# Kernel optimization log

Hardware: AMD Instinct MI355X
Metric: run time of the kernel (lower is better)

## Reference

```python
import jax, jax.numpy as jnp
import numpy as np

B, T, C, H = 2, 2048, 1024, 16

def setup_inputs() -> dict:
    key = jax.random.key(0)
    ks = jax.random.split(key, 6)
    s = 1.0 / np.sqrt(C)
    return {
        "x": jax.random.normal(ks[0], (B, T, C), jnp.float32),
        "Wq": jax.random.normal(ks[1], (C, C), jnp.float32) * s,
        "Wk": jax.random.normal(ks[2], (C, C), jnp.float32) * s,
        "Wv": jax.random.normal(ks[3], (C, C), jnp.float32) * s,
        "Wp": jax.random.normal(ks[4], (C, C), jnp.float32) * s,
        "bp": jnp.zeros((C,), jnp.float32),
    }

def reference(x, Wq, Wk, Wv, Wp, bp):
    b, t, c = x.shape
    hd = c // H  # head dim
    # Linear layers: torch nn.Linear computes x @ W.T
    def split_heads(y):
        return y.reshape(b, t, H, hd).transpose(0, 2, 1, 3)  # [B,H,T,hd]
    q = split_heads(x @ Wq.T)
    k = split_heads(x @ Wk.T)
    v = split_heads(x @ Wv.T)
    scale = hd ** -0.5
    wei = jnp.einsum('bhqd,bhkd->bhqk', q, k) * scale  # [B,H,T,T]
    causal = jnp.tril(jnp.ones((t, t), bool))
    wei = jnp.where(causal, wei, -jnp.inf)
    wei = jax.nn.softmax(wei, axis=-1)
    out = jnp.einsum('bhqk,bhkd->bhqd', wei, v)  # [B,H,T,hd]
    out = out.transpose(0, 2, 1, 3).reshape(b, t, c)
    return out @ Wp.T + bp
```

## Files before the change

### kernel.cpp

```cpp
#include <hip/hip_runtime.h>
#include <hip/hip_bf16.h>
#include <stdint.h>

#define B_ 2
#define T_ 2048
#define C_ 1024
#define H_ 16
#define HD_ 64
#define NTOK (B_*T_)

typedef __bf16 bf16;
typedef bf16 bf16x4 __attribute__((ext_vector_type(4)));
typedef bf16 bf16x8 __attribute__((ext_vector_type(8)));
typedef float f32x4 __attribute__((ext_vector_type(4)));

static __device__ __forceinline__ f32x4 mfma16(bf16x8 a, bf16x8 b, f32x4 c) {
  return __builtin_amdgcn_mfma_f32_16x16x32_bf16(a, b, c, 0, 0, 0);
}

static __device__ __forceinline__ void gload_lds16(const void* g, void* l) {
  __builtin_amdgcn_global_load_lds(
      (__attribute__((address_space(1))) void*)g,
      (__attribute__((address_space(3))) void*)l, 16, 0, 0);
}

static __device__ __forceinline__ uint32_t cvt_pk_bf16(float lo, float hi) {
  uint32_t r;
  asm("v_cvt_pk_bf16_f32 %0, %1, %2" : "=v"(r) : "v"(lo), "v"(hi));
  return r;
}

__global__ void cvt_all(const float* __restrict__ x,
                        const float* __restrict__ w0, const float* __restrict__ w1,
                        const float* __restrict__ w2, const float* __restrict__ w3,
                        bf16* __restrict__ xb,
                        bf16* __restrict__ d0, bf16* __restrict__ d1,
                        bf16* __restrict__ d2, bf16* __restrict__ d3) {
  const int i = blockIdx.x * 256 + threadIdx.x;
  const int y = blockIdx.y;
  const float* src;
  bf16* dst;
  size_t off4 = 0;
  if (y < 4) {
    src = x; dst = xb; off4 = (size_t)y << 18;
  } else if (y == 4) { src = w0; dst = d0; }
  else if (y == 5)   { src = w1; dst = d1; }
  else if (y == 6)   { src = w2; dst = d2; }
  else               { src = w3; dst = d3; }
  float4 v = reinterpret_cast<const float4*>(src)[off4 + i];
  bf16x4 o;
  o.x = (bf16)v.x; o.y = (bf16)v.y; o.z = (bf16)v.z; o.w = (bf16)v.w;
  reinterpret_cast<bf16x4*>(dst)[off4 + i] = o;
}

__global__ __launch_bounds__(256) void qkv_gemm(
    const bf16* __restrict__ X,
    const bf16* __restrict__ Wq, const bf16* __restrict__ Wk, const bf16* __restrict__ Wv,
    bf16* __restrict__ Q, bf16* __restrict__ K, bf16* __restrict__ VT) {
  __shared__ bf16 As[128 * 32];
  __shared__ bf16 Bs[128 * 32];
  const int z = blockIdx.z;
  const bf16* W = (z == 0) ? Wq : (z == 1) ? Wk : Wv;
  const int n0 = blockIdx.x * 128;
  const int o0 = blockIdx.y * 128;
  const int tid = threadIdx.x;
  const int lane = tid & 63;
  const int w = tid >> 6;
  const int wr = w >> 1, wc = w & 1;
  const int l15 = lane & 15, lhi = lane >> 4;

  f32x4 acc[4][4] = {};

  const int ca = tid;
  const int cb = tid + 256;
  const int rowa = ca >> 2, cola = (ca & 3) * 8;
  const int rowb = cb >> 2, colb = (cb & 3) * 8;

  for (int k0 = 0; k0 < C_; k0 += 32) {
    __syncthreads();
    gload_lds16(X + (size_t)(n0 + rowa) * C_ + k0 + cola, (char*)As + ca * 16);
    gload_lds16(X + (size_t)(n0 + rowb) * C_ + k0 + colb, (char*)As + cb * 16);
    gload_lds16(W + (size_t)(o0 + rowa) * C_ + k0 + cola, (char*)Bs + ca * 16);
    gload_lds16(W + (size_t)(o0 + rowb) * C_ + k0 + colb, (char*)Bs + cb * 16);
    __syncthreads();
    bf16x8 a[4], b[4];
#pragma unroll
    for (int m = 0; m < 4; m++)
      a[m] = *reinterpret_cast<const bf16x8*>(&As[(wr * 64 + m * 16 + l15) * 32 + lhi * 8]);
#pragma unroll
    for (int n = 0; n < 4; n++)
      b[n] = *reinterpret_cast<const bf16x8*>(&Bs[(wc * 64 + n * 16 + l15) * 32 + lhi * 8]);
#pragma unroll
    for (int m = 0; m < 4; m++)
#pragma unroll
      for (int n = 0; n < 4; n++)
        acc[m][n] = mfma16(a[m], b[n], acc[m][n]);
  }

  const float QSCALE = 0.125f * 1.44269504f;
#pragma unroll
  for (int m = 0; m < 4; m++) {
#pragma unroll
    for (int n = 0; n < 4; n++) {
#pragma unroll
      for (int r = 0; r < 4; r++) {
        int tok = n0 + wr * 64 + m * 16 + lhi * 4 + r;
        int o = o0 + wc * 64 + n * 16 + l15;
        int bb = tok >> 11, t = tok & (T_ - 1);
        int h = o >> 6, d = o & 63;
        float v = acc[m][n][r];
        if (z == 0) {
          Q[((size_t)(bb * H_ + h) * T_ + t) * HD_ + d] = (bf16)(v * QSCALE);
        } else if (z == 1) {
          K[((size_t)(bb * H_ + h) * T_ + t) * HD_ + d] = (bf16)v;
        } else {
          VT[((size_t)(bb * H_ + h) * HD_ + d) * T_ + t] = (bf16)v;
        }
      }
    }
  }
}

__global__ __launch_bounds__(256, 3) void attn_kernel(
    const bf16* __restrict__ Q, const bf16* __restrict__ K,
    const bf16* __restrict__ VT, bf16* __restrict__ att) {
  __shared__ bf16 Kt[2][64 * 64];
  __shared__ bf16 Vt[2][64 * 64];
  __shared__ bf16 P[4][32][72];
  const int tid = threadIdx.x;
  const int lane = tid & 63;
  const int w = tid >> 6;
  const int l15 = lane & 15, lhi = lane >> 4;
  const int bh = blockIdx.x;
  const int b = bh >> 4, h = bh & 15;
  const int by = (int)blockIdx.y;
  const int qt = (by < 8) ? (15 - by) : (by - 8);
  const int qw0 = qt * 128 + w * 32;
  const bf16* Qb = Q + (size_t)bh * T_ * HD_;
  const bf16* Kb = K + (size_t)bh * T_ * HD_;
  const bf16* Vb = VT + (size_t)bh * HD_ * T_;

  bf16x8 q[2][2];
#pragma unroll
  for (int m = 0; m < 2; m++)
#pragma unroll
    for (int kk = 0; kk < 2; kk++)
      q[m][kk] = *reinterpret_cast<const bf16x8*>(
          &Qb[(size_t)(qw0 + m * 16 + l15) * HD_ + kk * 32 + lhi * 8]);

  f32x4 o_acc[2][4] = {};
  float lsum[2] = {0.f, 0.f};

  const int nt = 2 * qt + 2;

  const int c0 = tid, c1 = tid + 256;
  const int r0 = c0 >> 3, x0 = (c0 & 7) ^ (r0 & 7);
  const int r1 = c1 >> 3, x1 = (c1 & 7) ^ (r1 & 7);

#define STAGE(tt, bb)                                                                \
  do {                                                                               \
    int kv = (tt) * 64;                                                              \
    gload_lds16(Kb + (size_t)(kv + r0) * HD_ + x0 * 8, (char*)&Kt[bb][0] + c0 * 16); \
    gload_lds16(Kb + (size_t)(kv + r1) * HD_ + x1 * 8, (char*)&Kt[bb][0] + c1 * 16); \
    gload_lds16(Vb + (size_t)r0 * T_ + kv + x0 * 8, (char*)&Vt[bb][0] + c0 * 16);    \
    gload_lds16(Vb + (size_t)r1 * T_ + kv + x1 * 8, (char*)&Vt[bb][0] + c1 * 16);    \
  } while (0)

  STAGE(0, 0);
  __syncthreads();
  int cur = 0;

  for (int it = 0; it < nt; ++it) {
    const int kv0 = it * 64;
    if (it + 1 < nt) STAGE(it + 1, cur ^ 1);

    if (kv0 <= qw0 + 31) {
      f32x4 s[2][4] = {};
#pragma unroll
      for (int n = 0; n < 4; n++) {
        const int krow = n * 16 + l15;
#pragma unroll
        for (int kk = 0; kk < 2; kk++) {
          const int kx = (kk * 4 + lhi) ^ (l15 & 7);
          bf16x8 kf = *reinterpret_cast<const bf16x8*>(
              (const char*)&Kt[cur][0] + krow * 128 + kx * 16);
          s[0][n] = mfma16(kf, q[0][kk], s[0][n]);
          s[1][n] = mfma16(kf, q[1][kk], s[1][n]);
        }
      }

      if (kv0 + 63 > qw0) {
#pragma unroll
        for (int m = 0; m < 2; m++) {
          const int qrow = qw0 + m * 16 + l15;
#pragma unroll
          for (int n = 0; n < 4; n++) {
            const int key = kv0 + n * 16 + lhi * 4;
#pragma unroll
            for (int r = 0; r < 4; r++) {
              if (key + r > qrow) s[m][n][r] = -1e30f;
            }
          }
        }
      }
#pragma unroll
      for (int m = 0; m < 2; m++) {
        char* pw = (char*)&P[w][m * 16 + l15][0];
#pragma unroll
        for (int n = 0; n < 4; n++) {
          float p0 = __builtin_amdgcn_exp2f(s[m][n][0]);
          float p1 = __builtin_amdgcn_exp2f(s[m][n][1]);
          float p2 = __builtin_amdgcn_exp2f(s[m][n][2]);
          float p3 = __builtin_amdgcn_exp2f(s[m][n][3]);
          lsum[m] += (p0 + p1) + (p2 + p3);
          uint32_t lo = cvt_pk_bf16(p0, p1);
          uint32_t hi = cvt_pk_bf16(p2, p3);
          *reinterpret_cast<uint2*>(pw + (4 * n + lhi) * 8) = make_uint2(lo, hi);
        }
      }
      bf16x8 pa[2][2];
#pragma unroll
      for (int m = 0; m < 2; m++)
#pragma unroll
        for (int kk = 0; kk < 2; kk++)
          pa[m][kk] = *reinterpret_cast<const bf16x8*>(
              (const char*)&P[w][m * 16 + l15][0] + kk * 64 + lhi * 16);
#pragma unroll
      for (int n = 0; n < 4; n++) {
        const int vrow = n * 16 + l15;
#pragma unroll
        for (int kk = 0; kk < 2; kk++) {
          const int vx = (kk * 4 + lhi) ^ (l15 & 7);
          bf16x8 vf = *reinterpret_cast<const bf16x8*>(
              (const char*)&Vt[cur][0] + vrow * 128 + vx * 16);
          o_acc[0][n] = mfma16(pa[0][kk], vf, o_acc[0][n]);
          o_acc[1][n] = mfma16(pa[1][kk], vf, o_acc[1][n]);
        }
      }
    }
    __syncthreads();
    cur ^= 1;
  }
#undef STAGE

  float lred[2];
#pragma unroll
  for (int m = 0; m < 2; m++) {
    float v = lsum[m];
    v += __shfl_xor(v, 16);
    v += __shfl_xor(v, 32);
    lred[m] = v;
  }
#pragma unroll
  for (int m = 0; m < 2; m++) {
#pragma unroll
    for (int r = 0; r < 4; r++) {
      float rs = __shfl(lred[m], (lane & 48) + lhi * 4 + r);
      float li = 1.f / rs;
      int t = qw0 + m * 16 + lhi * 4 + r;
#pragma unroll
      for (int n = 0; n < 4; n++) {
        int d = n * 16 + l15;
        att[((size_t)(b * T_ + t) * H_ + h) * HD_ + d] = (bf16)(o_acc[m][n][r] * li);
      }
    }
  }
}

__global__ __launch_bounds__(256) void proj_gemm(
    const bf16* __restrict__ A, const bf16* __restrict__ Wp,
    const float* __restrict__ bp, float* __restrict__ out) {
  __shared__ bf16 As[128 * 32];
  __shared__ bf16 Bs[128 * 32];
  const int n0 = blockIdx.x * 128;
  const int o0 = blockIdx.y * 128;
  const int tid = threadIdx.x;
  const int lane = tid & 63;
  const int w = tid >> 6;
  const int wr = w >> 1, wc = w & 1;
  const int l15 = lane & 15, lhi = lane >> 4;

  f32x4 acc[4][4] = {};

  const int ca = tid;
  const int cb = tid + 256;
  const int rowa = ca >> 2, cola = (ca & 3) * 8;
  const int rowb = cb >> 2, colb = (cb & 3) * 8;

  for (int k0 = 0; k0 < C_; k0 += 32) {
    __syncthreads();
    gload_lds16(A + (size_t)(n0 + rowa) * C_ + k0 + cola, (char*)As + ca * 16);
    gload_lds16(A + (size_t)(n0 + rowb) * C_ + k0 + colb, (char*)As + cb * 16);
    gload_lds16(Wp + (size_t)(o0 + rowa) * C_ + k0 + cola, (char*)Bs + ca * 16);
    gload_lds16(Wp + (size_t)(o0 + rowb) * C_ + k0 + colb, (char*)Bs + cb * 16);
    __syncthreads();
    bf16x8 a[4], b[4];
#pragma unroll
    for (int m = 0; m < 4; m++)
      a[m] = *reinterpret_cast<const bf16x8*>(&As[(wr * 64 + m * 16 + l15) * 32 + lhi * 8]);
#pragma unroll
    for (int n = 0; n < 4; n++)
      b[n] = *reinterpret_cast<const bf16x8*>(&Bs[(wc * 64 + n * 16 + l15) * 32 + lhi * 8]);
#pragma unroll
    for (int m = 0; m < 4; m++)
#pragma unroll
      for (int n = 0; n < 4; n++)
        acc[m][n] = mfma16(a[m], b[n], acc[m][n]);
  }

#pragma unroll
  for (int m = 0; m < 4; m++) {
#pragma unroll
    for (int n = 0; n < 4; n++) {
#pragma unroll
      for (int r = 0; r < 4; r++) {
        int tok = n0 + wr * 64 + m * 16 + lhi * 4 + r;
        int o = o0 + wc * 64 + n * 16 + l15;
        out[(size_t)tok * C_ + o] = acc[m][n][r] + bp[o];
      }
    }
  }
}

extern "C" void kernel_launch(void* const* d_in, const int* in_sizes, int n_in,
                              void* d_out, int out_size, void* d_ws, size_t ws_size,
                              hipStream_t stream) {
  const float* x  = (const float*)d_in[0];
  const float* Wq = (const float*)d_in[1];
  const float* Wk = (const float*)d_in[2];
  const float* Wv = (const float*)d_in[3];
  const float* Wp = (const float*)d_in[4];
  const float* bp = (const float*)d_in[5];
  float* out = (float*)d_out;

  char* ws = (char*)d_ws;
  size_t off = 0;
  bf16* xb  = (bf16*)(ws + off); off += (size_t)NTOK * C_ * 2;
  bf16* wqb = (bf16*)(ws + off); off += (size_t)C_ * C_ * 2;
  bf16* wkb = (bf16*)(ws + off); off += (size_t)C_ * C_ * 2;
  bf16* wvb = (bf16*)(ws + off); off += (size_t)C_ * C_ * 2;
  bf16* wpb = (bf16*)(ws + off); off += (size_t)C_ * C_ * 2;
  bf16* Qd  = (bf16*)(ws + off); off += (size_t)NTOK * C_ * 2;
  bf16* Kd  = (bf16*)(ws + off); off += (size_t)NTOK * C_ * 2;
  bf16* VTd = (bf16*)(ws + off); off += (size_t)NTOK * C_ * 2;
  bf16* att = (bf16*)(ws + off); off += (size_t)NTOK * C_ * 2;
  (void)ws_size; (void)out_size; (void)in_sizes; (void)n_in;

  cvt_all<<<dim3(1024, 8), 256, 0, stream>>>(x, Wq, Wk, Wv, Wp, xb, wqb, wkb, wvb, wpb);

  qkv_gemm<<<dim3(NTOK / 128, C_ / 128, 3), 256, 0, stream>>>(xb, wqb, wkb, wvb, Qd, Kd, VTd);
  attn_kernel<<<dim3(B_ * H_, 16), 256, 0, stream>>>(Qd, Kd, VTd, att);
  proj_gemm<<<dim3(NTOK / 128, C_ / 128), 256, 0, stream>>>(att, wpb, bp, out);
}
```

Baseline: 113.0 us.

## Rewrite QKV GEMM with 256x192 tiles, double-buffered swizzled LDS and interleaved loads

Rewrites the fused QKV projection as one GEMM over the concatenated weights. This relies on the Q, K and V weight buffers sitting next to each other in the workspace. Each 512-thread block computes a 256x192 tile with K steps of 64. Next-step loads go into an XOR-swizzled, double-buffered LDS and are spread across four MFMA phases with priority hints, so global loads hide behind compute. The aim is to fix the old kernel's single-buffered, two-barrier loop with its small K step. In exchange it uses more LDS and registers, and the final prefetch reads past the end of each row into neighbouring memory, which is harmless.

```diff
diff --git a/kernel.cpp b/kernel.cpp
--- a/kernel.cpp
+++ b/kernel.cpp
@@ -29,6 +29,9 @@
   asm("v_cvt_pk_bf16_f32 %0, %1, %2" : "=v"(r) : "v"(lo), "v"(hi));
   return r;
 }
+
+#define BAR() do { __builtin_amdgcn_sched_barrier(0); __builtin_amdgcn_s_barrier(); __builtin_amdgcn_sched_barrier(0); } while (0)
+#define BARV0() do { asm volatile("s_waitcnt vmcnt(0)"); __builtin_amdgcn_sched_barrier(0); __builtin_amdgcn_s_barrier(); __builtin_amdgcn_sched_barrier(0); } while (0)
 
 __global__ void cvt_all(const float* __restrict__ x,
                         const float* __restrict__ w0, const float* __restrict__ w1,
@@ -53,62 +56,141 @@
   reinterpret_cast<bf16x4*>(dst)[off4 + i] = o;
 }
 
-__global__ __launch_bounds__(256) void qkv_gemm(
-    const bf16* __restrict__ X,
-    const bf16* __restrict__ Wq, const bf16* __restrict__ Wk, const bf16* __restrict__ Wv,
+__global__ __launch_bounds__(512) void qkv_gemm(
+    const bf16* __restrict__ X, const bf16* __restrict__ Wcat,
     bf16* __restrict__ Q, bf16* __restrict__ K, bf16* __restrict__ VT) {
-  __shared__ bf16 As[128 * 32];
-  __shared__ bf16 Bs[128 * 32];
-  const int z = blockIdx.z;
-  const bf16* W = (z == 0) ? Wq : (z == 1) ? Wk : Wv;
-  const int n0 = blockIdx.x * 128;
-  const int o0 = blockIdx.y * 128;
+  __shared__ bf16 As[2][256 * 64];
+  __shared__ bf16 Bs[2][192 * 64];
   const int tid = threadIdx.x;
   const int lane = tid & 63;
-  const int w = tid >> 6;
-  const int wr = w >> 1, wc = w & 1;
+  const int wid = tid >> 6;
+  const int wm = wid >> 2, wn = wid & 3;
   const int l15 = lane & 15, lhi = lane >> 4;
-
-  f32x4 acc[4][4] = {};
-
-  const int ca = tid;
-  const int cb = tid + 256;
-  const int rowa = ca >> 2, cola = (ca & 3) * 8;
-  const int rowb = cb >> 2, colb = (cb & 3) * 8;
-
-  for (int k0 = 0; k0 < C_; k0 += 32) {
-    __syncthreads();
-    gload_lds16(X + (size_t)(n0 + rowa) * C_ + k0 + cola, (char*)As + ca * 16);
-    gload_lds16(X + (size_t)(n0 + rowb) * C_ + k0 + colb, (char*)As + cb * 16);
-    gload_lds16(W + (size_t)(o0 + rowa) * C_ + k0 + cola, (char*)Bs + ca * 16);
-    gload_lds16(W + (size_t)(o0 + rowb) * C_ + k0 + colb, (char*)Bs + cb * 16);
-    __syncthreads();
-    bf16x8 a[4], b[4];
-#pragma unroll
-    for (int m = 0; m < 4; m++)
-      a[m] = *reinterpret_cast<const bf16x8*>(&As[(wr * 64 + m * 16 + l15) * 32 + lhi * 8]);
-#pragma unroll
-    for (int n = 0; n < 4; n++)
-      b[n] = *reinterpret_cast<const bf16x8*>(&Bs[(wc * 64 + n * 16 + l15) * 32 + lhi * 8]);
-#pragma unroll
-    for (int m = 0; m < 4; m++)
-#pragma unroll
-      for (int n = 0; n < 4; n++)
-        acc[m][n] = mfma16(a[m], b[n], acc[m][n]);
-  }
+  const int M0 = blockIdx.x * 256;
+  const int N0 = blockIdx.y * 192;
+  const int sr = tid >> 3;
+  const int ss = tid & 7;
+
+  f32x4 acc[8][3] = {};
+
+#define STAGE_A(kt, d, h)                                                          \
+  do {                                                                             \
+    _Pragma("unroll")                                                              \
+    for (int j = 0; j < 2; j++) {                                                  \
+      int row = (h) * 128 + sr + j * 64;                                           \
+      gload_lds16(X + (size_t)(M0 + row) * C_ + (kt) * 64 + ((ss ^ (row & 7)) * 8),\
+                  (char*)&As[d][0] + row * 128 + ss * 16);                         \
+    }                                                                              \
+  } while (0)
+
+#define STAGE_B(kt, d, c)                                                          \
+  do {                                                                             \
+    int row = (c) * 64 + sr;                                                       \
+    gload_lds16(Wcat + (size_t)(N0 + row) * C_ + (kt) * 64 + ((ss ^ (row & 7)) * 8),\
+                (char*)&Bs[d][0] + row * 128 + ss * 16);                           \
+  } while (0)
+
+  STAGE_A(0, 0, 0); STAGE_A(0, 0, 1);
+  STAGE_B(0, 0, 0); STAGE_B(0, 0, 1); STAGE_B(0, 0, 2);
+  BARV0();
+
+  bf16x8 a[8][2], b[3][2];
+
+  for (int T = 0; T < 16; ++T) {
+    const int cur = T & 1, nxt = cur ^ 1;
+    const int kn = T + 1;
+
+    STAGE_A(kn, nxt, 0);
+#pragma unroll
+    for (int mf = 0; mf < 4; mf++) {
+      const int row = wm * 128 + mf * 16 + l15;
+#pragma unroll
+      for (int kk = 0; kk < 2; kk++)
+        a[mf][kk] = *reinterpret_cast<const bf16x8*>(
+            (const char*)&As[cur][0] + row * 128 + (((kk * 4 + lhi) ^ (row & 7)) * 16));
+    }
+#pragma unroll
+    for (int nf = 0; nf < 2; nf++) {
+      const int row = wn * 48 + nf * 16 + l15;
+#pragma unroll
+      for (int kk = 0; kk < 2; kk++)
+        b[nf][kk] = *reinterpret_cast<const bf16x8*>(
+            (const char*)&Bs[cur][0] + row * 128 + (((kk * 4 + lhi) ^ (row & 7)) * 16));
+    }
+    __builtin_amdgcn_s_setprio(1);
+#pragma unroll
+    for (int mf = 0; mf < 4; mf++)
+#pragma unroll
+      for (int nf = 0; nf < 2; nf++)
+#pragma unroll
+        for (int kk = 0; kk < 2; kk++)
+          acc[mf][nf] = mfma16(a[mf][kk], b[nf][kk], acc[mf][nf]);
+    __builtin_amdgcn_s_setprio(0);
+    BAR();
+
+    STAGE_A(kn, nxt, 1);
+    {
+      const int row = wn * 48 + 2 * 16 + l15;
+#pragma unroll
+      for (int kk = 0; kk < 2; kk++)
+        b[2][kk] = *reinterpret_cast<const bf16x8*>(
+            (const char*)&Bs[cur][0] + row * 128 + (((kk * 4 + lhi) ^ (row & 7)) * 16));
+    }
+    __builtin_amdgcn_s_setprio(1);
+#pragma unroll
+    for (int mf = 0; mf < 4; mf++)
+#pragma unroll
+      for (int kk = 0; kk < 2; kk++)
+        acc[mf][2] = mfma16(a[mf][kk], b[2][kk], acc[mf][2]);
+    __builtin_amdgcn_s_setprio(0);
+    BAR();
+
+    STAGE_B(kn, nxt, 0); STAGE_B(kn, nxt, 1);
+#pragma unroll
+    for (int mf = 4; mf < 8; mf++) {
+      const int row = wm * 128 + mf * 16 + l15;
+#pragma unroll
+      for (int kk = 0; kk < 2; kk++)
+        a[mf][kk] = *reinterpret_cast<const bf16x8*>(
+            (const char*)&As[cur][0] + row * 128 + (((kk * 4 + lhi) ^ (row & 7)) * 16));
+    }
+    __builtin_amdgcn_s_setprio(1);
+#pragma unroll
+    for (int mf = 4; mf < 8; mf++)
+#pragma unroll
+      for (int kk = 0; kk < 2; kk++)
+        acc[mf][2] = mfma16(a[mf][kk], b[2][kk], acc[mf][2]);
+    __builtin_amdgcn_s_setprio(0);
+    BAR();
+
+    STAGE_B(kn, nxt, 2);
+    __builtin_amdgcn_s_setprio(1);
+#pragma unroll
+    for (int mf = 4; mf < 8; mf++)
+#pragma unroll
+      for (int nf = 0; nf < 2; nf++)
+#pragma unroll
+        for (int kk = 0; kk < 2; kk++)
+          acc[mf][nf] = mfma16(a[mf][kk], b[nf][kk], acc[mf][nf]);
+    __builtin_amdgcn_s_setprio(0);
+    BARV0();
+  }
+#undef STAGE_A
+#undef STAGE_B
 
   const float QSCALE = 0.125f * 1.44269504f;
 #pragma unroll
-  for (int m = 0; m < 4; m++) {
-#pragma unroll
-    for (int n = 0; n < 4; n++) {
+  for (int mf = 0; mf < 8; mf++) {
+#pragma unroll
+    for (int nf = 0; nf < 3; nf++) {
 #pragma unroll
       for (int r = 0; r < 4; r++) {
-        int tok = n0 + wr * 64 + m * 16 + lhi * 4 + r;
-        int o = o0 + wc * 64 + n * 16 + l15;
+        int tok = M0 + wm * 128 + mf * 16 + lhi * 4 + r;
+        int o = N0 + wn * 48 + nf * 16 + l15;
+        int z = o >> 10, oz = o & 1023;
+        int h = oz >> 6, d = oz & 63;
         int bb = tok >> 11, t = tok & (T_ - 1);
-        int h = o >> 6, d = o & 63;
-        float v = acc[m][n][r];
+        float v = acc[mf][nf][r];
         if (z == 0) {
           Q[((size_t)(bb * H_ + h) * T_ + t) * HD_ + d] = (bf16)(v * QSCALE);
         } else if (z == 1) {
@@ -348,7 +430,7 @@
 
   cvt_all<<<dim3(1024, 8), 256, 0, stream>>>(x, Wq, Wk, Wv, Wp, xb, wqb, wkb, wvb, wpb);
 
-  qkv_gemm<<<dim3(NTOK / 128, C_ / 128, 3), 256, 0, stream>>>(xb, wqb, wkb, wvb, Qd, Kd, VTd);
+  qkv_gemm<<<dim3(16, 16), 512, 0, stream>>>(xb, wqb, Qd, Kd, VTd);
   attn_kernel<<<dim3(B_ * H_, 16), 256, 0, stream>>>(Qd, Kd, VTd, att);
   proj_gemm<<<dim3(NTOK / 128, C_ / 128), 256, 0, stream>>>(att, wpb, bp, out);
 }
```

Measured after the change: 132.0 us. +16.9%, slower.
